# Performance work log

Measured on AMD Instinct MI355X. Metric: run time of the kernel, lower is better.

Reference implementation:

```python
import jax, jax.numpy as jnp
import numpy as np

N_NODES = 2000   # buses per graph = state_dim // 2
K_HOPS = 3       # TAGConv K
HIDDEN = 64
F_NODE = 2       # node_feat_dim
B_DIM, W_DIM = 8, 32


def setup_inputs() -> dict:
    key = jax.random.key(0)
    ks = jax.random.split(key, 4)
    N = N_NODES
    rng = np.random.default_rng(0)
    # sparse symmetric ybus sparsity: chain + random chords (power-grid like, avg degree ~4)
    ii = np.arange(N - 1)
    jj = ii + 1
    ci = np.arange(N)
    cj = (ci + rng.integers(2, N - 1, size=N)) % N
    src = np.concatenate([ii, ci])
    dst = np.concatenate([jj, cj])
    row = np.concatenate([src, dst]).astype(np.int32)   # symmetrized: both directions
    col = np.concatenate([dst, src]).astype(np.int32)
    w = rng.uniform(0.5, 2.0, size=src.shape[0]).astype(np.float32)  # |ybus| entries
    ew = np.concatenate([w, w]).astype(np.float32)
    x = jax.random.normal(ks[0], (B_DIM, W_DIM, 2 * N), dtype=jnp.float32)
    # TAGConv params: K+1 weight matrices (no per-lin bias in PyG TAGConv lins) + one bias
    W1 = jax.random.normal(ks[1], (K_HOPS + 1, F_NODE, HIDDEN), dtype=jnp.float32) * (1.0 / np.sqrt(F_NODE))
    b1 = jnp.zeros((HIDDEN,), jnp.float32)
    W2 = jax.random.normal(ks[2], (K_HOPS + 1, HIDDEN, F_NODE), dtype=jnp.float32) * (1.0 / np.sqrt(HIDDEN))
    b2 = jnp.zeros((F_NODE,), jnp.float32)
    return {"x": x, "row": jnp.asarray(row), "col": jnp.asarray(col),
            "ew": jnp.asarray(ew), "W1": W1, "b1": b1, "W2": W2, "b2": b2}


def _propagate(x, row, col, norm, N):
    # x: [G, N, F]; gather at source, weight, scatter-add at target
    msg = x[:, row, :] * norm[None, :, None]                       # [G, E, F]
    return jax.vmap(lambda m: jax.ops.segment_sum(m, col, num_segments=N))(msg)


def _tag_conv(x, Ws, b, row, col, norm, N):
    # TAGConv: out = sum_k lin_k(A_hat^k x) + b
    out = jnp.einsum('gnf,fo->gno', x, Ws[0])
    h = x
    for k in range(1, Ws.shape[0]):
        h = _propagate(h, row, col, norm, N)
        out = out + jnp.einsum('gnf,fo->gno', h, Ws[k])
    return out + b


def reference(x, row, col, ew, W1, b1, W2, b2):
    B, Wd, twoN = x.shape
    N = twoN // 2
    G = B * Wd
    xn = x.reshape(G, N, F_NODE)
    # gcn_norm (add_self_loops=False), shared across all tiled graphs
    deg = jax.ops.segment_sum(ew, col, num_segments=N)
    safe = jnp.where(deg > 0, deg, 1.0)
    dinv = jnp.where(deg > 0, 1.0 / jnp.sqrt(safe), 0.0)
    norm = dinv[row] * ew * dinv[col]
    h = _tag_conv(xn, W1, b1, row, col, norm, N)
    h = jax.nn.relu(h)
    h = _tag_conv(h, W2, b2, row, col, norm, N)
    out = xn + h  # residual refine
    return out.reshape(B, Wd, twoN)
```

## Files before the change

kernel.cpp:

```cpp
#include <hip/hip_runtime.h>
#include <math.h>


#define NN    2000
#define HID   64
#define TPB   1024
#define BKCAP 12

typedef float v2f __attribute__((ext_vector_type(2)));

struct NodeAdj {
    int   l, r, c;
    float wl, wr, wc;
    int   m0, m1, m2, m3;
    float w0, w1, w2, w3;
    int   tail0, tail1;
    float dn;
};

__device__ __forceinline__ v2f gather2(const v2f* __restrict__ buf,
                                       const NodeAdj& A,
                                       const unsigned short* __restrict__ bkt16,
                                       const float* __restrict__ ewc,
                                       const float* __restrict__ dinvL)
{
    v2f acc0 = A.wl * buf[A.l];
    v2f acc1 = A.wr * buf[A.r];
    acc0 += A.wc * buf[A.c];
    acc1 += A.w0 * buf[A.m0];
    acc0 += A.w1 * buf[A.m1];
    acc1 += A.w2 * buf[A.m2];
    acc0 += A.w3 * buf[A.m3];
    for (int p = A.tail0; p < A.tail1; ++p) {
        int m = bkt16[p];
        float w = A.dn * ewc[m] * dinvL[m];
        acc1 += w * buf[m];
    }
    return acc0 + acc1;
}

__global__ __launch_bounds__(TPB) void refine_kernel(
    const float* __restrict__ x,
    const int*   __restrict__ row, const int* __restrict__ col,
    const float* __restrict__ ew,
    const float* __restrict__ W1, const float* __restrict__ b1,
    const float* __restrict__ W2, const float* __restrict__ b2,
    float* __restrict__ out)
{
    __shared__ int            cnt[NN];
    __shared__ unsigned short bkt16[NN * BKCAP];
    __shared__ float          ewc[NN];
    __shared__ float          dinvL[NN];
    __shared__ v2f            bufP[NN];
    __shared__ v2f            bufQ[NN];

    const int g = blockIdx.x;
    const int t = threadIdx.x;
    const int n0 = t;
    const int n1 = t + TPB;
    const bool has1 = (n1 < NN);
    const float* xg   = x   + (size_t)g * (2 * NN);
    float*       outg = out + (size_t)g * (2 * NN);

    float y[2][8];
    v2f Zp[2][4];
#pragma unroll
    for (int q = 0; q < 8; ++q) { y[0][q] = 0.f; y[1][q] = 0.f; }
#pragma unroll
    for (int q = 0; q < 4; ++q) { Zp[0][q] = (v2f)0.f; Zp[1][q] = (v2f)0.f; }

    cnt[t] = 0;
    if (t + TPB < NN) cnt[t + TPB] = 0;
    ewc[n0] = ew[(NN - 1) + n0];
    if (has1) ewc[n1] = ew[(NN - 1) + n1];
    {
        v2f v = ((const v2f*)xg)[n0];
        bufP[n0] = v; y[0][0] = v.x; y[0][1] = v.y;
        if (has1) {
            v2f u = ((const v2f*)xg)[n1];
            bufP[n1] = u; y[1][0] = u.x; y[1][1] = u.y;
        }
    }
    const int cA = col[(NN - 1) + n0];
    const float ewlA = (n0 > 0)      ? ew[n0 - 1] : 0.f;
    const float ewrA = (n0 < NN - 1) ? ew[n0]     : 0.f;
    int cB = 0; float ewlB = 0.f, ewrB = 0.f;
    if (has1) {
        cB   = col[(NN - 1) + n1];
        ewlB = ew[n1 - 1];
        ewrB = (n1 < NN - 1) ? ew[n1] : 0.f;
    }
    __syncthreads();

    {
        int pos = atomicAdd(&cnt[cA], 1);
        if (pos < BKCAP) bkt16[cA * BKCAP + pos] = (unsigned short)n0;
        if (has1) {
            int pos1 = atomicAdd(&cnt[cB], 1);
            if (pos1 < BKCAP) bkt16[cB * BKCAP + pos1] = (unsigned short)n1;
        }
    }
    __syncthreads();

    int bdA = cnt[n0]; if (bdA > BKCAP) bdA = BKCAP;
    const int baseA = n0 * BKCAP;
    int mA0 = 0, mA1 = 0, mA2 = 0, mA3 = 0;
    float eA0 = 0.f, eA1 = 0.f, eA2 = 0.f, eA3 = 0.f;
    {
        float deg = ewc[n0] + ewlA + ewrA;
        if (bdA > 0) { mA0 = bkt16[baseA];     eA0 = ewc[mA0]; deg += eA0; }
        if (bdA > 1) { mA1 = bkt16[baseA + 1]; eA1 = ewc[mA1]; deg += eA1; }
        if (bdA > 2) { mA2 = bkt16[baseA + 2]; eA2 = ewc[mA2]; deg += eA2; }
        if (bdA > 3) { mA3 = bkt16[baseA + 3]; eA3 = ewc[mA3]; deg += eA3; }
        for (int k = 4; k < bdA; ++k) deg += ewc[bkt16[baseA + k]];
        dinvL[n0] = 1.0f / sqrtf(deg);
    }
    int bdB = 0, baseB = 0;
    int mB0 = 0, mB1 = 0, mB2 = 0, mB3 = 0;
    float eB0 = 0.f, eB1 = 0.f, eB2 = 0.f, eB3 = 0.f;
    if (has1) {
        bdB = cnt[n1]; if (bdB > BKCAP) bdB = BKCAP;
        baseB = n1 * BKCAP;
        float deg = ewc[n1] + ewlB + ewrB;
        if (bdB > 0) { mB0 = bkt16[baseB];     eB0 = ewc[mB0]; deg += eB0; }
        if (bdB > 1) { mB1 = bkt16[baseB + 1]; eB1 = ewc[mB1]; deg += eB1; }
        if (bdB > 2) { mB2 = bkt16[baseB + 2]; eB2 = ewc[mB2]; deg += eB2; }
        if (bdB > 3) { mB3 = bkt16[baseB + 3]; eB3 = ewc[mB3]; deg += eB3; }
        for (int k = 4; k < bdB; ++k) deg += ewc[bkt16[baseB + k]];
        dinvL[n1] = 1.0f / sqrtf(deg);
    }
    __syncthreads();

    NodeAdj A, B;
    {
        float dn = dinvL[n0];
        A.l = (n0 > 0) ? n0 - 1 : 0;
        A.r = (n0 < NN - 1) ? n0 + 1 : NN - 1;
        A.c = cA;
        A.wl = dn * ewlA * dinvL[A.l];
        A.wr = dn * ewrA * dinvL[A.r];
        A.wc = dn * ewc[n0] * dinvL[cA];
        A.m0 = mA0; A.m1 = mA1; A.m2 = mA2; A.m3 = mA3;
        A.w0 = dn * eA0 * dinvL[mA0];
        A.w1 = dn * eA1 * dinvL[mA1];
        A.w2 = dn * eA2 * dinvL[mA2];
        A.w3 = dn * eA3 * dinvL[mA3];
        A.tail0 = baseA + 4;
        A.tail1 = baseA + ((bdA > 4) ? bdA : 4);
        A.dn = dn;
    }
    B.l = 0; B.r = 0; B.c = 0; B.wl = 0.f; B.wr = 0.f; B.wc = 0.f;
    B.m0 = 0; B.m1 = 0; B.m2 = 0; B.m3 = 0;
    B.w0 = 0.f; B.w1 = 0.f; B.w2 = 0.f; B.w3 = 0.f;
    B.tail0 = 0; B.tail1 = 0; B.dn = 0.f;
    if (has1) {
        float dn = dinvL[n1];
        B.l = n1 - 1;
        B.r = (n1 < NN - 1) ? n1 + 1 : NN - 1;
        B.c = cB;
        B.wl = dn * ewlB * dinvL[B.l];
        B.wr = dn * ewrB * dinvL[B.r];
        B.wc = dn * ewc[n1] * dinvL[cB];
        B.m0 = mB0; B.m1 = mB1; B.m2 = mB2; B.m3 = mB3;
        B.w0 = dn * eB0 * dinvL[mB0];
        B.w1 = dn * eB1 * dinvL[mB1];
        B.w2 = dn * eB2 * dinvL[mB2];
        B.w3 = dn * eB3 * dinvL[mB3];
        B.tail0 = baseB + 4;
        B.tail1 = baseB + ((bdB > 4) ? bdB : 4);
        B.dn = dn;
    }

    v2f ra, rb;

    ra = gather2(bufP, A, bkt16, ewc, dinvL);
    if (has1) rb = gather2(bufP, B, bkt16, ewc, dinvL);
    y[0][2] = ra.x; y[0][3] = ra.y; bufQ[n0] = ra;
    if (has1) { y[1][2] = rb.x; y[1][3] = rb.y; bufQ[n1] = rb; }
    __syncthreads();

    ra = gather2(bufQ, A, bkt16, ewc, dinvL);
    if (has1) rb = gather2(bufQ, B, bkt16, ewc, dinvL);
    y[0][4] = ra.x; y[0][5] = ra.y; bufP[n0] = ra;
    if (has1) { y[1][4] = rb.x; y[1][5] = rb.y; bufP[n1] = rb; }
    __syncthreads();

    ra = gather2(bufP, A, bkt16, ewc, dinvL);
    if (has1) rb = gather2(bufP, B, bkt16, ewc, dinvL);
    y[0][6] = ra.x; y[0][7] = ra.y;
    if (has1) { y[1][6] = rb.x; y[1][7] = rb.y; }

    const v2f*    W1p = (const v2f*)W1;
    const v2f*    b1p = (const v2f*)b1;
    const float4* W2q = (const float4*)W2;
#pragma unroll 2
    for (int jh = 0; jh < HID / 2; ++jh) {
        v2f w1c[8];
#pragma unroll
        for (int m = 0; m < 8; ++m) w1c[m] = W1p[m * (HID / 2) + jh];
        v2f bj = b1p[jh];
        float4 w2a = W2q[0 * (HID / 2) + jh];
        float4 w2b = W2q[1 * (HID / 2) + jh];
        float4 w2c = W2q[2 * (HID / 2) + jh];
        float4 w2d = W2q[3 * (HID / 2) + jh];
        v2f wa_l = {w2a.x, w2a.y}, wa_h = {w2a.z, w2a.w};
        v2f wb_l = {w2b.x, w2b.y}, wb_h = {w2b.z, w2b.w};
        v2f wc_l = {w2c.x, w2c.y}, wc_h = {w2c.z, w2c.w};
        v2f wd_l = {w2d.x, w2d.y}, wd_h = {w2d.z, w2d.w};
#pragma unroll
        for (int i = 0; i < 2; ++i) {
            v2f ha = bj          + y[i][0] * w1c[0];
            v2f hb = y[i][1] * w1c[1] + y[i][2] * w1c[2];
            ha += y[i][3] * w1c[3];
            hb += y[i][4] * w1c[4];
            ha += y[i][5] * w1c[5];
            hb += y[i][6] * w1c[6];
            ha += y[i][7] * w1c[7];
            v2f h = ha + hb;
            float h0 = fmaxf(h.x, 0.f);
            float h1 = fmaxf(h.y, 0.f);
            Zp[i][0] += h0 * wa_l; Zp[i][0] += h1 * wa_h;
            Zp[i][1] += h0 * wb_l; Zp[i][1] += h1 * wb_h;
            Zp[i][2] += h0 * wc_l; Zp[i][2] += h1 * wc_h;
            Zp[i][3] += h0 * wd_l; Zp[i][3] += h1 * wd_h;
        }
    }

    bufQ[n0] = Zp[0][3];
    if (has1) bufQ[n1] = Zp[1][3];
    __syncthreads();

    ra = gather2(bufQ, A, bkt16, ewc, dinvL);
    if (has1) rb = gather2(bufQ, B, bkt16, ewc, dinvL);
    bufP[n0] = Zp[0][2] + ra;
    if (has1) bufP[n1] = Zp[1][2] + rb;
    __syncthreads();

    ra = gather2(bufP, A, bkt16, ewc, dinvL);
    if (has1) rb = gather2(bufP, B, bkt16, ewc, dinvL);
    bufQ[n0] = Zp[0][1] + ra;
    if (has1) bufQ[n1] = Zp[1][1] + rb;
    __syncthreads();

    const v2f b2v = {b2[0], b2[1]};
    ra = gather2(bufQ, A, bkt16, ewc, dinvL);
    if (has1) rb = gather2(bufQ, B, bkt16, ewc, dinvL);
    {
        v2f x0 = {y[0][0], y[0][1]};
        v2f o = x0 + b2v + Zp[0][0] + ra;
        ((v2f*)outg)[n0] = o;
        if (has1) {
            v2f x1 = {y[1][0], y[1][1]};
            v2f u = x1 + b2v + Zp[1][0] + rb;
            ((v2f*)outg)[n1] = u;
        }
    }
}

extern "C" void kernel_launch(void* const* d_in, const int* in_sizes, int n_in,
                              void* d_out, int out_size, void* d_ws, size_t ws_size,
                              hipStream_t stream) {
    const float* x   = (const float*)d_in[0];
    const int*   row = (const int*)  d_in[1];
    const int*   col = (const int*)  d_in[2];
    const float* ew  = (const float*)d_in[3];
    const float* W1  = (const float*)d_in[4];
    const float* b1  = (const float*)d_in[5];
    const float* W2  = (const float*)d_in[6];
    const float* b2  = (const float*)d_in[7];
    float* out = (float*)d_out;

    const int G = in_sizes[0] / (2 * NN);

    hipLaunchKernelGGL(refine_kernel, dim3(G), dim3(TPB), 0, stream,
                       x, row, col, ew, W1, b1, W2, b2, out);
}
```

Before: 102.5 us.

## Assign adjacent node pairs per thread with register-forwarded chain neighbours

Each thread now owns two adjacent nodes (2t, 2t+1) instead of nodes t and t+1024. The chain edge between the pair is served from registers (prevA/prevB), which removes one LDS gather per node per hop. Loads and stores of x, the buffers and the output widen to 16-byte vectors. In exchange, 1000 of 1024 threads are active, and the first-wave and second-wave workloads are no longer split, which may change latency hiding.

```diff
diff --git a/kernel.cpp b/kernel.cpp
--- a/kernel.cpp
+++ b/kernel.cpp
@@ -6,8 +6,10 @@
 #define HID   64
 #define TPB   1024
 #define BKCAP 12
+#define HALF  (NN / 2)
 
 typedef float v2f __attribute__((ext_vector_type(2)));
+typedef float v4f __attribute__((ext_vector_type(4)));
 
 struct NodeAdj {
     int   l, r, c;
@@ -18,25 +20,39 @@
     float dn;
 };
 
-__device__ __forceinline__ v2f gather2(const v2f* __restrict__ buf,
-                                       const NodeAdj& A,
-                                       const unsigned short* __restrict__ bkt16,
-                                       const float* __restrict__ ewc,
-                                       const float* __restrict__ dinvL)
+__device__ __forceinline__ void gatherPair(
+    const v2f* __restrict__ buf,
+    const NodeAdj& A, const NodeAdj& B,
+    v2f prevA, v2f prevB,
+    const unsigned short* __restrict__ bkt16,
+    const float* __restrict__ ewc,
+    const float* __restrict__ dinvL,
+    v2f& outA, v2f& outB)
 {
-    v2f acc0 = A.wl * buf[A.l];
-    v2f acc1 = A.wr * buf[A.r];
-    acc0 += A.wc * buf[A.c];
-    acc1 += A.w0 * buf[A.m0];
-    acc0 += A.w1 * buf[A.m1];
-    acc1 += A.w2 * buf[A.m2];
-    acc0 += A.w3 * buf[A.m3];
+    v2f a0 = A.wl * buf[A.l];
+    v2f a1 = A.wr * prevB;
+    v2f b0 = B.wl * prevA;
+    v2f b1 = B.wr * buf[B.r];
+    a0 += A.wc * buf[A.c];
+    b0 += B.wc * buf[B.c];
+    a1 += A.w0 * buf[A.m0];
+    b1 += B.w0 * buf[B.m0];
+    a0 += A.w1 * buf[A.m1];
+    b0 += B.w1 * buf[B.m1];
+    a1 += A.w2 * buf[A.m2];
+    b1 += B.w2 * buf[B.m2];
+    a0 += A.w3 * buf[A.m3];
+    b0 += B.w3 * buf[B.m3];
     for (int p = A.tail0; p < A.tail1; ++p) {
         int m = bkt16[p];
-        float w = A.dn * ewc[m] * dinvL[m];
-        acc1 += w * buf[m];
-    }
-    return acc0 + acc1;
+        a1 += (A.dn * ewc[m] * dinvL[m]) * buf[m];
+    }
+    for (int p = B.tail0; p < B.tail1; ++p) {
+        int m = bkt16[p];
+        b1 += (B.dn * ewc[m] * dinvL[m]) * buf[m];
+    }
+    outA = a0 + a1;
+    outB = b0 + b1;
 }
 
 __global__ __launch_bounds__(TPB) void refine_kernel(
@@ -47,18 +63,18 @@
     const float* __restrict__ W2, const float* __restrict__ b2,
     float* __restrict__ out)
 {
-    __shared__ int            cnt[NN];
-    __shared__ unsigned short bkt16[NN * BKCAP];
-    __shared__ float          ewc[NN];
-    __shared__ float          dinvL[NN];
-    __shared__ v2f            bufP[NN];
-    __shared__ v2f            bufQ[NN];
+    __shared__ int                          cnt[NN];
+    __shared__ unsigned short               bkt16[NN * BKCAP];
+    __shared__ __align__(16) float          ewc[NN];
+    __shared__ __align__(16) float          dinvL[NN];
+    __shared__ __align__(16) v2f            bufP[NN];
+    __shared__ __align__(16) v2f            bufQ[NN];
 
     const int g = blockIdx.x;
     const int t = threadIdx.x;
-    const int n0 = t;
-    const int n1 = t + TPB;
-    const bool has1 = (n1 < NN);
+    const bool act = (t < HALF);
+    const int n0 = 2 * t;
+    const int n1 = 2 * t + 1;
     const float* xg   = x   + (size_t)g * (2 * NN);
     float*       outg = out + (size_t)g * (2 * NN);
 
@@ -68,192 +84,197 @@
     for (int q = 0; q < 8; ++q) { y[0][q] = 0.f; y[1][q] = 0.f; }
 #pragma unroll
     for (int q = 0; q < 4; ++q) { Zp[0][q] = (v2f)0.f; Zp[1][q] = (v2f)0.f; }
+    v2f prevA = (v2f)0.f, prevB = (v2f)0.f;
 
     cnt[t] = 0;
     if (t + TPB < NN) cnt[t + TPB] = 0;
-    ewc[n0] = ew[(NN - 1) + n0];
-    if (has1) ewc[n1] = ew[(NN - 1) + n1];
-    {
-        v2f v = ((const v2f*)xg)[n0];
-        bufP[n0] = v; y[0][0] = v.x; y[0][1] = v.y;
-        if (has1) {
-            v2f u = ((const v2f*)xg)[n1];
-            bufP[n1] = u; y[1][0] = u.x; y[1][1] = u.y;
-        }
-    }
-    const int cA = col[(NN - 1) + n0];
-    const float ewlA = (n0 > 0)      ? ew[n0 - 1] : 0.f;
-    const float ewrA = (n0 < NN - 1) ? ew[n0]     : 0.f;
-    int cB = 0; float ewlB = 0.f, ewrB = 0.f;
-    if (has1) {
-        cB   = col[(NN - 1) + n1];
-        ewlB = ew[n1 - 1];
-        ewrB = (n1 < NN - 1) ? ew[n1] : 0.f;
-    }
-    __syncthreads();
-
-    {
+    int   cA = 0, cB = 0;
+    float ewl = 0.f, ewm = 0.f, ewr = 0.f;
+    float ecA = 0.f, ecB = 0.f;
+    if (act) {
+        ecA = ew[(NN - 1) + n0];
+        ecB = ew[(NN - 1) + n1];
+        ((float2*)ewc)[t] = make_float2(ecA, ecB);
+        v4f v = ((const v4f*)xg)[t];
+        ((v4f*)bufP)[t] = v;
+        y[0][0] = v.x; y[0][1] = v.y; y[1][0] = v.z; y[1][1] = v.w;
+        prevA = (v2f){v.x, v.y};
+        prevB = (v2f){v.z, v.w};
+        cA = col[(NN - 1) + n0];
+        cB = col[(NN - 1) + n1];
+        ewl = (n0 > 0) ? ew[n0 - 1] : 0.f;
+        ewm = ew[n0];
+        ewr = (n1 < NN - 1) ? ew[n1] : 0.f;
+    }
+    __syncthreads();
+
+    if (act) {
         int pos = atomicAdd(&cnt[cA], 1);
         if (pos < BKCAP) bkt16[cA * BKCAP + pos] = (unsigned short)n0;
-        if (has1) {
-            int pos1 = atomicAdd(&cnt[cB], 1);
-            if (pos1 < BKCAP) bkt16[cB * BKCAP + pos1] = (unsigned short)n1;
+        int pos1 = atomicAdd(&cnt[cB], 1);
+        if (pos1 < BKCAP) bkt16[cB * BKCAP + pos1] = (unsigned short)n1;
+    }
+    __syncthreads();
+
+    const int baseA = n0 * BKCAP, baseB = n1 * BKCAP;
+    int bdA = 0, bdB = 0;
+    int mA0 = 0, mA1 = 0, mA2 = 0, mA3 = 0;
+    int mB0 = 0, mB1 = 0, mB2 = 0, mB3 = 0;
+    float eA0 = 0.f, eA1 = 0.f, eA2 = 0.f, eA3 = 0.f;
+    float eB0 = 0.f, eB1 = 0.f, eB2 = 0.f, eB3 = 0.f;
+    float dnA = 0.f, dnB = 0.f;
+    if (act) {
+        bdA = cnt[n0]; if (bdA > BKCAP) bdA = BKCAP;
+        {
+            float deg = ecA + ewl + ewm;
+            if (bdA > 0) { mA0 = bkt16[baseA];     eA0 = ewc[mA0]; deg += eA0; }
+            if (bdA > 1) { mA1 = bkt16[baseA + 1]; eA1 = ewc[mA1]; deg += eA1; }
+            if (bdA > 2) { mA2 = bkt16[baseA + 2]; eA2 = ewc[mA2]; deg += eA2; }
+            if (bdA > 3) { mA3 = bkt16[baseA + 3]; eA3 = ewc[mA3]; deg += eA3; }
+            for (int k = 4; k < bdA; ++k) deg += ewc[bkt16[baseA + k]];
+            dnA = 1.0f / sqrtf(deg);
         }
-    }
-    __syncthreads();
-
-    int bdA = cnt[n0]; if (bdA > BKCAP) bdA = BKCAP;
-    const int baseA = n0 * BKCAP;
-    int mA0 = 0, mA1 = 0, mA2 = 0, mA3 = 0;
-    float eA0 = 0.f, eA1 = 0.f, eA2 = 0.f, eA3 = 0.f;
-    {
-        float deg = ewc[n0] + ewlA + ewrA;
-        if (bdA > 0) { mA0 = bkt16[baseA];     eA0 = ewc[mA0]; deg += eA0; }
-        if (bdA > 1) { mA1 = bkt16[baseA + 1]; eA1 = ewc[mA1]; deg += eA1; }
-        if (bdA > 2) { mA2 = bkt16[baseA + 2]; eA2 = ewc[mA2]; deg += eA2; }
-        if (bdA > 3) { mA3 = bkt16[baseA + 3]; eA3 = ewc[mA3]; deg += eA3; }
-        for (int k = 4; k < bdA; ++k) deg += ewc[bkt16[baseA + k]];
-        dinvL[n0] = 1.0f / sqrtf(deg);
-    }
-    int bdB = 0, baseB = 0;
-    int mB0 = 0, mB1 = 0, mB2 = 0, mB3 = 0;
-    float eB0 = 0.f, eB1 = 0.f, eB2 = 0.f, eB3 = 0.f;
-    if (has1) {
         bdB = cnt[n1]; if (bdB > BKCAP) bdB = BKCAP;
-        baseB = n1 * BKCAP;
-        float deg = ewc[n1] + ewlB + ewrB;
-        if (bdB > 0) { mB0 = bkt16[baseB];     eB0 = ewc[mB0]; deg += eB0; }
-        if (bdB > 1) { mB1 = bkt16[baseB + 1]; eB1 = ewc[mB1]; deg += eB1; }
-        if (bdB > 2) { mB2 = bkt16[baseB + 2]; eB2 = ewc[mB2]; deg += eB2; }
-        if (bdB > 3) { mB3 = bkt16[baseB + 3]; eB3 = ewc[mB3]; deg += eB3; }
-        for (int k = 4; k < bdB; ++k) deg += ewc[bkt16[baseB + k]];
-        dinvL[n1] = 1.0f / sqrtf(deg);
+        {
+            float deg = ecB + ewm + ewr;
+            if (bdB > 0) { mB0 = bkt16[baseB];     eB0 = ewc[mB0]; deg += eB0; }
+            if (bdB > 1) { mB1 = bkt16[baseB + 1]; eB1 = ewc[mB1]; deg += eB1; }
+            if (bdB > 2) { mB2 = bkt16[baseB + 2]; eB2 = ewc[mB2]; deg += eB2; }
+            if (bdB > 3) { mB3 = bkt16[baseB + 3]; eB3 = ewc[mB3]; deg += eB3; }
+            for (int k = 4; k < bdB; ++k) deg += ewc[bkt16[baseB + k]];
+            dnB = 1.0f / sqrtf(deg);
+        }
+        ((float2*)dinvL)[t] = make_float2(dnA, dnB);
     }
     __syncthreads();
 
     NodeAdj A, B;
-    {
-        float dn = dinvL[n0];
+    A.l = 0; A.r = 0; A.c = 0; A.wl = 0.f; A.wr = 0.f; A.wc = 0.f;
+    A.m0 = 0; A.m1 = 0; A.m2 = 0; A.m3 = 0;
+    A.w0 = 0.f; A.w1 = 0.f; A.w2 = 0.f; A.w3 = 0.f;
+    A.tail0 = 0; A.tail1 = 0; A.dn = 0.f;
+    B = A;
+    if (act) {
         A.l = (n0 > 0) ? n0 - 1 : 0;
-        A.r = (n0 < NN - 1) ? n0 + 1 : NN - 1;
         A.c = cA;
-        A.wl = dn * ewlA * dinvL[A.l];
-        A.wr = dn * ewrA * dinvL[A.r];
-        A.wc = dn * ewc[n0] * dinvL[cA];
+        A.wl = dnA * ewl * dinvL[A.l];
+        A.wr = dnA * ewm * dnB;
+        A.wc = dnA * ecA * dinvL[cA];
         A.m0 = mA0; A.m1 = mA1; A.m2 = mA2; A.m3 = mA3;
-        A.w0 = dn * eA0 * dinvL[mA0];
-        A.w1 = dn * eA1 * dinvL[mA1];
-        A.w2 = dn * eA2 * dinvL[mA2];
-        A.w3 = dn * eA3 * dinvL[mA3];
+        A.w0 = dnA * eA0 * dinvL[mA0];
+        A.w1 = dnA * eA1 * dinvL[mA1];
+        A.w2 = dnA * eA2 * dinvL[mA2];
+        A.w3 = dnA * eA3 * dinvL[mA3];
         A.tail0 = baseA + 4;
         A.tail1 = baseA + ((bdA > 4) ? bdA : 4);
-        A.dn = dn;
-    }
-    B.l = 0; B.r = 0; B.c = 0; B.wl = 0.f; B.wr = 0.f; B.wc = 0.f;
-    B.m0 = 0; B.m1 = 0; B.m2 = 0; B.m3 = 0;
-    B.w0 = 0.f; B.w1 = 0.f; B.w2 = 0.f; B.w3 = 0.f;
-    B.tail0 = 0; B.tail1 = 0; B.dn = 0.f;
-    if (has1) {
-        float dn = dinvL[n1];
-        B.l = n1 - 1;
+        A.dn = dnA;
+
         B.r = (n1 < NN - 1) ? n1 + 1 : NN - 1;
         B.c = cB;
-        B.wl = dn * ewlB * dinvL[B.l];
-        B.wr = dn * ewrB * dinvL[B.r];
-        B.wc = dn * ewc[n1] * dinvL[cB];
+        B.wl = dnB * ewm * dnA;
+        B.wr = dnB * ewr * dinvL[B.r];
+        B.wc = dnB * ecB * dinvL[cB];
         B.m0 = mB0; B.m1 = mB1; B.m2 = mB2; B.m3 = mB3;
-        B.w0 = dn * eB0 * dinvL[mB0];
-        B.w1 = dn * eB1 * dinvL[mB1];
-        B.w2 = dn * eB2 * dinvL[mB2];
-        B.w3 = dn * eB3 * dinvL[mB3];
+        B.w0 = dnB * eB0 * dinvL[mB0];
+        B.w1 = dnB * eB1 * dinvL[mB1];
+        B.w2 = dnB * eB2 * dinvL[mB2];
+        B.w3 = dnB * eB3 * dinvL[mB3];
         B.tail0 = baseB + 4;
         B.tail1 = baseB + ((bdB > 4) ? bdB : 4);
-        B.dn = dn;
+        B.dn = dnB;
     }
 
     v2f ra, rb;
 
-    ra = gather2(bufP, A, bkt16, ewc, dinvL);
-    if (has1) rb = gather2(bufP, B, bkt16, ewc, dinvL);
-    y[0][2] = ra.x; y[0][3] = ra.y; bufQ[n0] = ra;
-    if (has1) { y[1][2] = rb.x; y[1][3] = rb.y; bufQ[n1] = rb; }
-    __syncthreads();
-
-    ra = gather2(bufQ, A, bkt16, ewc, dinvL);
-    if (has1) rb = gather2(bufQ, B, bkt16, ewc, dinvL);
-    y[0][4] = ra.x; y[0][5] = ra.y; bufP[n0] = ra;
-    if (has1) { y[1][4] = rb.x; y[1][5] = rb.y; bufP[n1] = rb; }
-    __syncthreads();
-
-    ra = gather2(bufP, A, bkt16, ewc, dinvL);
-    if (has1) rb = gather2(bufP, B, bkt16, ewc, dinvL);
-    y[0][6] = ra.x; y[0][7] = ra.y;
-    if (has1) { y[1][6] = rb.x; y[1][7] = rb.y; }
-
-    const v2f*    W1p = (const v2f*)W1;
-    const v2f*    b1p = (const v2f*)b1;
-    const float4* W2q = (const float4*)W2;
+    if (act) {
+        gatherPair(bufP, A, B, prevA, prevB, bkt16, ewc, dinvL, ra, rb);
+        y[0][2] = ra.x; y[0][3] = ra.y; y[1][2] = rb.x; y[1][3] = rb.y;
+        ((v4f*)bufQ)[t] = (v4f){ra.x, ra.y, rb.x, rb.y};
+        prevA = ra; prevB = rb;
+    }
+    __syncthreads();
+
+    if (act) {
+        gatherPair(bufQ, A, B, prevA, prevB, bkt16, ewc, dinvL, ra, rb);
+        y[0][4] = ra.x; y[0][5] = ra.y; y[1][4] = rb.x; y[1][5] = rb.y;
+        ((v4f*)bufP)[t] = (v4f){ra.x, ra.y, rb.x, rb.y};
+        prevA = ra; prevB = rb;
+    }
+    __syncthreads();
+
+    if (act) {
+        gatherPair(bufP, A, B, prevA, prevB, bkt16, ewc, dinvL, ra, rb);
+        y[0][6] = ra.x; y[0][7] = ra.y; y[1][6] = rb.x; y[1][7] = rb.y;
+    }
+
+    if (act) {
+        const v2f*    W1p = (const v2f*)W1;
+        const v2f*    b1p = (const v2f*)b1;
+        const float4* W2q = (const float4*)W2;
 #pragma unroll 2
-    for (int jh = 0; jh < HID / 2; ++jh) {
-        v2f w1c[8];
-#pragma unroll
-        for (int m = 0; m < 8; ++m) w1c[m] = W1p[m * (HID / 2) + jh];
-        v2f bj = b1p[jh];
-        float4 w2a = W2q[0 * (HID / 2) + jh];
-        float4 w2b = W2q[1 * (HID / 2) + jh];
-        float4 w2c = W2q[2 * (HID / 2) + jh];
-        float4 w2d = W2q[3 * (HID / 2) + jh];
-        v2f wa_l = {w2a.x, w2a.y}, wa_h = {w2a.z, w2a.w};
-        v2f wb_l = {w2b.x, w2b.y}, wb_h = {w2b.z, w2b.w};
-        v2f wc_l = {w2c.x, w2c.y}, wc_h = {w2c.z, w2c.w};
-        v2f wd_l = {w2d.x, w2d.y}, wd_h = {w2d.z, w2d.w};
-#pragma unroll
-        for (int i = 0; i < 2; ++i) {
-            v2f ha = bj          + y[i][0] * w1c[0];
-            v2f hb = y[i][1] * w1c[1] + y[i][2] * w1c[2];
-            ha += y[i][3] * w1c[3];
-            hb += y[i][4] * w1c[4];
-            ha += y[i][5] * w1c[5];
-            hb += y[i][6] * w1c[6];
-            ha += y[i][7] * w1c[7];
-            v2f h = ha + hb;
-            float h0 = fmaxf(h.x, 0.f);
-            float h1 = fmaxf(h.y, 0.f);
-            Zp[i][0] += h0 * wa_l; Zp[i][0] += h1 * wa_h;
-            Zp[i][1] += h0 * wb_l; Zp[i][1] += h1 * wb_h;
-            Zp[i][2] += h0 * wc_l; Zp[i][2] += h1 * wc_h;
-            Zp[i][3] += h0 * wd_l; Zp[i][3] += h1 * wd_h;
+        for (int jh = 0; jh < HID / 2; ++jh) {
+            v2f w1c[8];
+#pragma unroll
+            for (int m = 0; m < 8; ++m) w1c[m] = W1p[m * (HID / 2) + jh];
+            v2f bj = b1p[jh];
+            float4 w2a = W2q[0 * (HID / 2) + jh];
+            float4 w2b = W2q[1 * (HID / 2) + jh];
+            float4 w2c = W2q[2 * (HID / 2) + jh];
+            float4 w2d = W2q[3 * (HID / 2) + jh];
+            v2f wa_l = {w2a.x, w2a.y}, wa_h = {w2a.z, w2a.w};
+            v2f wb_l = {w2b.x, w2b.y}, wb_h = {w2b.z, w2b.w};
+            v2f wc_l = {w2c.x, w2c.y}, wc_h = {w2c.z, w2c.w};
+            v2f wd_l = {w2d.x, w2d.y}, wd_h = {w2d.z, w2d.w};
+#pragma unroll
+            for (int i = 0; i < 2; ++i) {
+                v2f ha = bj          + y[i][0] * w1c[0];
+                v2f hb = y[i][1] * w1c[1] + y[i][2] * w1c[2];
+                ha += y[i][3] * w1c[3];
+                hb += y[i][4] * w1c[4];
+                ha += y[i][5] * w1c[5];
+                hb += y[i][6] * w1c[6];
+                ha += y[i][7] * w1c[7];
+                v2f h = ha + hb;
+                float h0 = fmaxf(h.x, 0.f);
+                float h1 = fmaxf(h.y, 0.f);
+                Zp[i][0] += h0 * wa_l; Zp[i][0] += h1 * wa_h;
+                Zp[i][1] += h0 * wb_l; Zp[i][1] += h1 * wb_h;
+                Zp[i][2] += h0 * wc_l; Zp[i][2] += h1 * wc_h;
+                Zp[i][3] += h0 * wd_l; Zp[i][3] += h1 * wd_h;
+            }
         }
     }
 
-    bufQ[n0] = Zp[0][3];
-    if (has1) bufQ[n1] = Zp[1][3];
-    __syncthreads();
-
-    ra = gather2(bufQ, A, bkt16, ewc, dinvL);
-    if (has1) rb = gather2(bufQ, B, bkt16, ewc, dinvL);
-    bufP[n0] = Zp[0][2] + ra;
-    if (has1) bufP[n1] = Zp[1][2] + rb;
-    __syncthreads();
-
-    ra = gather2(bufP, A, bkt16, ewc, dinvL);
-    if (has1) rb = gather2(bufP, B, bkt16, ewc, dinvL);
-    bufQ[n0] = Zp[0][1] + ra;
-    if (has1) bufQ[n1] = Zp[1][1] + rb;
-    __syncthreads();
-
-    const v2f b2v = {b2[0], b2[1]};
-    ra = gather2(bufQ, A, bkt16, ewc, dinvL);
-    if (has1) rb = gather2(bufQ, B, bkt16, ewc, dinvL);
-    {
+    if (act) {
+        ((v4f*)bufQ)[t] = (v4f){Zp[0][3].x, Zp[0][3].y, Zp[1][3].x, Zp[1][3].y};
+        prevA = Zp[0][3]; prevB = Zp[1][3];
+    }
+    __syncthreads();
+
+    if (act) {
+        gatherPair(bufQ, A, B, prevA, prevB, bkt16, ewc, dinvL, ra, rb);
+        v2f sA = Zp[0][2] + ra, sB = Zp[1][2] + rb;
+        ((v4f*)bufP)[t] = (v4f){sA.x, sA.y, sB.x, sB.y};
+        prevA = sA; prevB = sB;
+    }
+    __syncthreads();
+
+    if (act) {
+        gatherPair(bufP, A, B, prevA, prevB, bkt16, ewc, dinvL, ra, rb);
+        v2f sA = Zp[0][1] + ra, sB = Zp[1][1] + rb;
+        ((v4f*)bufQ)[t] = (v4f){sA.x, sA.y, sB.x, sB.y};
+        prevA = sA; prevB = sB;
+    }
+    __syncthreads();
+
+    if (act) {
+        const v2f b2v = {b2[0], b2[1]};
+        gatherPair(bufQ, A, B, prevA, prevB, bkt16, ewc, dinvL, ra, rb);
         v2f x0 = {y[0][0], y[0][1]};
-        v2f o = x0 + b2v + Zp[0][0] + ra;
-        ((v2f*)outg)[n0] = o;
-        if (has1) {
-            v2f x1 = {y[1][0], y[1][1]};
-            v2f u = x1 + b2v + Zp[1][0] + rb;
-            ((v2f*)outg)[n1] = u;
-        }
+        v2f x1 = {y[1][0], y[1][1]};
+        v2f oA = x0 + b2v + Zp[0][0] + ra;
+        v2f oB = x1 + b2v + Zp[1][0] + rb;
+        ((v4f*)outg)[t] = (v4f){oA.x, oA.y, oB.x, oB.y};
     }
 }
 
```

Result: slower. 112.4 us (+9.7%).

## Precompute normalized adjacency once in a separate build kernel

Applied to the files above, without the earlier changes.

Before this change, each of the 256 graph blocks rebuilt the bucketed adjacency and gcn normalization in large shared memory. Now a single-block build kernel writes packed per-node neighbor indices and weights to workspace. The refine kernel then only loads them as float4/int4 and keeps small shared buffers. This removes redundant per-block setup and shrinks LDS use, which may allow more blocks per CU. The cost is an extra serial kernel launch and global reads in the tail loop.

```diff
diff --git a/kernel.cpp b/kernel.cpp
--- a/kernel.cpp
+++ b/kernel.cpp
@@ -11,18 +11,16 @@
 
 struct NodeAdj {
     int   l, r, c;
+    int   m0, m1, m2, m3;
     float wl, wr, wc;
-    int   m0, m1, m2, m3;
     float w0, w1, w2, w3;
-    int   tail0, tail1;
-    float dn;
+    int   tbase, tc;
 };
 
 __device__ __forceinline__ v2f gather2(const v2f* __restrict__ buf,
                                        const NodeAdj& A,
-                                       const unsigned short* __restrict__ bkt16,
-                                       const float* __restrict__ ewc,
-                                       const float* __restrict__ dinvL)
+                                       const int* __restrict__ adjtm,
+                                       const float* __restrict__ adjtw)
 {
     v2f acc0 = A.wl * buf[A.l];
     v2f acc1 = A.wr * buf[A.r];
@@ -31,56 +29,33 @@
     acc0 += A.w1 * buf[A.m1];
     acc1 += A.w2 * buf[A.m2];
     acc0 += A.w3 * buf[A.m3];
-    for (int p = A.tail0; p < A.tail1; ++p) {
-        int m = bkt16[p];
-        float w = A.dn * ewc[m] * dinvL[m];
+    for (int p = 0; p < A.tc; ++p) {
+        int   m = adjtm[A.tbase + p];
+        float w = adjtw[A.tbase + p];
         acc1 += w * buf[m];
     }
     return acc0 + acc1;
 }
 
-__global__ __launch_bounds__(TPB) void refine_kernel(
-    const float* __restrict__ x,
-    const int*   __restrict__ row, const int* __restrict__ col,
-    const float* __restrict__ ew,
-    const float* __restrict__ W1, const float* __restrict__ b1,
-    const float* __restrict__ W2, const float* __restrict__ b2,
-    float* __restrict__ out)
+__global__ __launch_bounds__(TPB) void build_kernel(
+    const int* __restrict__ col, const float* __restrict__ ew,
+    float* __restrict__ adjw, int* __restrict__ adji,
+    float* __restrict__ adjtw, int* __restrict__ adjtm)
 {
     __shared__ int            cnt[NN];
     __shared__ unsigned short bkt16[NN * BKCAP];
     __shared__ float          ewc[NN];
     __shared__ float          dinvL[NN];
-    __shared__ v2f            bufP[NN];
-    __shared__ v2f            bufQ[NN];
-
-    const int g = blockIdx.x;
+
     const int t = threadIdx.x;
     const int n0 = t;
     const int n1 = t + TPB;
     const bool has1 = (n1 < NN);
-    const float* xg   = x   + (size_t)g * (2 * NN);
-    float*       outg = out + (size_t)g * (2 * NN);
-
-    float y[2][8];
-    v2f Zp[2][4];
-#pragma unroll
-    for (int q = 0; q < 8; ++q) { y[0][q] = 0.f; y[1][q] = 0.f; }
-#pragma unroll
-    for (int q = 0; q < 4; ++q) { Zp[0][q] = (v2f)0.f; Zp[1][q] = (v2f)0.f; }
 
     cnt[t] = 0;
     if (t + TPB < NN) cnt[t + TPB] = 0;
     ewc[n0] = ew[(NN - 1) + n0];
     if (has1) ewc[n1] = ew[(NN - 1) + n1];
-    {
-        v2f v = ((const v2f*)xg)[n0];
-        bufP[n0] = v; y[0][0] = v.x; y[0][1] = v.y;
-        if (has1) {
-            v2f u = ((const v2f*)xg)[n1];
-            bufP[n1] = u; y[1][0] = u.x; y[1][1] = u.y;
-        }
-    }
     const int cA = col[(NN - 1) + n0];
     const float ewlA = (n0 > 0)      ? ew[n0 - 1] : 0.f;
     const float ewrA = (n0 < NN - 1) ? ew[n0]     : 0.f;
@@ -131,62 +106,135 @@
     }
     __syncthreads();
 
+    {
+        float dn = dinvL[n0];
+        int l = (n0 > 0) ? n0 - 1 : 0;
+        int r = (n0 < NN - 1) ? n0 + 1 : NN - 1;
+        float4* wp = (float4*)(adjw + n0 * 8);
+        wp[0] = make_float4(dn * ewlA * dinvL[l],
+                            dn * ewrA * dinvL[r],
+                            dn * ewc[n0] * dinvL[cA],
+                            dn * eA0 * dinvL[mA0]);
+        wp[1] = make_float4(dn * eA1 * dinvL[mA1],
+                            dn * eA2 * dinvL[mA2],
+                            dn * eA3 * dinvL[mA3], 0.f);
+        int4* ip = (int4*)(adji + n0 * 8);
+        ip[0] = make_int4(cA, mA0, mA1, mA2);
+        ip[1] = make_int4(mA3, bdA, 0, 0);
+        int tc = (bdA > 4) ? bdA - 4 : 0;
+        for (int k = 0; k < tc; ++k) {
+            int m = bkt16[baseA + 4 + k];
+            adjtm[n0 * 8 + k] = m;
+            adjtw[n0 * 8 + k] = dn * ewc[m] * dinvL[m];
+        }
+    }
+    if (has1) {
+        float dn = dinvL[n1];
+        int l = n1 - 1;
+        int r = (n1 < NN - 1) ? n1 + 1 : NN - 1;
+        float4* wp = (float4*)(adjw + n1 * 8);
+        wp[0] = make_float4(dn * ewlB * dinvL[l],
+                            dn * ewrB * dinvL[r],
+                            dn * ewc[n1] * dinvL[cB],
+                            dn * eB0 * dinvL[mB0]);
+        wp[1] = make_float4(dn * eB1 * dinvL[mB1],
+                            dn * eB2 * dinvL[mB2],
+                            dn * eB3 * dinvL[mB3], 0.f);
+        int4* ip = (int4*)(adji + n1 * 8);
+        ip[0] = make_int4(cB, mB0, mB1, mB2);
+        ip[1] = make_int4(mB3, bdB, 0, 0);
+        int tc = (bdB > 4) ? bdB - 4 : 0;
+        for (int k = 0; k < tc; ++k) {
+            int m = bkt16[baseB + 4 + k];
+            adjtm[n1 * 8 + k] = m;
+            adjtw[n1 * 8 + k] = dn * ewc[m] * dinvL[m];
+        }
+    }
+}
+
+__global__ __launch_bounds__(TPB) void refine_kernel(
+    const float* __restrict__ x,
+    const float* __restrict__ W1, const float* __restrict__ b1,
+    const float* __restrict__ W2, const float* __restrict__ b2,
+    const float* __restrict__ adjw, const int* __restrict__ adji,
+    const float* __restrict__ adjtw, const int* __restrict__ adjtm,
+    float* __restrict__ out)
+{
+    __shared__ v2f bufP[NN];
+    __shared__ v2f bufQ[NN];
+
+    const int g = blockIdx.x;
+    const int t = threadIdx.x;
+    const int n0 = t;
+    const int n1 = t + TPB;
+    const bool has1 = (n1 < NN);
+    const float* xg   = x   + (size_t)g * (2 * NN);
+    float*       outg = out + (size_t)g * (2 * NN);
+
+    float y[2][8];
+    v2f Zp[2][4];
+#pragma unroll
+    for (int q = 0; q < 8; ++q) { y[0][q] = 0.f; y[1][q] = 0.f; }
+#pragma unroll
+    for (int q = 0; q < 4; ++q) { Zp[0][q] = (v2f)0.f; Zp[1][q] = (v2f)0.f; }
+
+    {
+        v2f v = ((const v2f*)xg)[n0];
+        bufP[n0] = v; y[0][0] = v.x; y[0][1] = v.y;
+        if (has1) {
+            v2f u = ((const v2f*)xg)[n1];
+            bufP[n1] = u; y[1][0] = u.x; y[1][1] = u.y;
+        }
+    }
     NodeAdj A, B;
     {
-        float dn = dinvL[n0];
+        float4 w0 = ((const float4*)(adjw))[n0 * 2];
+        float4 w1 = ((const float4*)(adjw))[n0 * 2 + 1];
+        int4   i0 = ((const int4*)(adji))[n0 * 2];
+        int4   i1 = ((const int4*)(adji))[n0 * 2 + 1];
         A.l = (n0 > 0) ? n0 - 1 : 0;
         A.r = (n0 < NN - 1) ? n0 + 1 : NN - 1;
-        A.c = cA;
-        A.wl = dn * ewlA * dinvL[A.l];
-        A.wr = dn * ewrA * dinvL[A.r];
-        A.wc = dn * ewc[n0] * dinvL[cA];
-        A.m0 = mA0; A.m1 = mA1; A.m2 = mA2; A.m3 = mA3;
-        A.w0 = dn * eA0 * dinvL[mA0];
-        A.w1 = dn * eA1 * dinvL[mA1];
-        A.w2 = dn * eA2 * dinvL[mA2];
-        A.w3 = dn * eA3 * dinvL[mA3];
-        A.tail0 = baseA + 4;
-        A.tail1 = baseA + ((bdA > 4) ? bdA : 4);
-        A.dn = dn;
-    }
-    B.l = 0; B.r = 0; B.c = 0; B.wl = 0.f; B.wr = 0.f; B.wc = 0.f;
-    B.m0 = 0; B.m1 = 0; B.m2 = 0; B.m3 = 0;
+        A.c = i0.x; A.m0 = i0.y; A.m1 = i0.z; A.m2 = i0.w; A.m3 = i1.x;
+        A.wl = w0.x; A.wr = w0.y; A.wc = w0.z; A.w0 = w0.w;
+        A.w1 = w1.x; A.w2 = w1.y; A.w3 = w1.z;
+        A.tbase = n0 * 8;
+        A.tc = (i1.y > 4) ? i1.y - 4 : 0;
+    }
+    B.l = 0; B.r = 0; B.c = 0; B.m0 = 0; B.m1 = 0; B.m2 = 0; B.m3 = 0;
+    B.wl = 0.f; B.wr = 0.f; B.wc = 0.f;
     B.w0 = 0.f; B.w1 = 0.f; B.w2 = 0.f; B.w3 = 0.f;
-    B.tail0 = 0; B.tail1 = 0; B.dn = 0.f;
+    B.tbase = 0; B.tc = 0;
     if (has1) {
-        float dn = dinvL[n1];
+        float4 w0 = ((const float4*)(adjw))[n1 * 2];
+        float4 w1 = ((const float4*)(adjw))[n1 * 2 + 1];
+        int4   i0 = ((const int4*)(adji))[n1 * 2];
+        int4   i1 = ((const int4*)(adji))[n1 * 2 + 1];
         B.l = n1 - 1;
         B.r = (n1 < NN - 1) ? n1 + 1 : NN - 1;
-        B.c = cB;
-        B.wl = dn * ewlB * dinvL[B.l];
-        B.wr = dn * ewrB * dinvL[B.r];
-        B.wc = dn * ewc[n1] * dinvL[cB];
-        B.m0 = mB0; B.m1 = mB1; B.m2 = mB2; B.m3 = mB3;
-        B.w0 = dn * eB0 * dinvL[mB0];
-        B.w1 = dn * eB1 * dinvL[mB1];
-        B.w2 = dn * eB2 * dinvL[mB2];
-        B.w3 = dn * eB3 * dinvL[mB3];
-        B.tail0 = baseB + 4;
-        B.tail1 = baseB + ((bdB > 4) ? bdB : 4);
-        B.dn = dn;
-    }
+        B.c = i0.x; B.m0 = i0.y; B.m1 = i0.z; B.m2 = i0.w; B.m3 = i1.x;
+        B.wl = w0.x; B.wr = w0.y; B.wc = w0.z; B.w0 = w0.w;
+        B.w1 = w1.x; B.w2 = w1.y; B.w3 = w1.z;
+        B.tbase = n1 * 8;
+        B.tc = (i1.y > 4) ? i1.y - 4 : 0;
+    }
+    __syncthreads();
 
     v2f ra, rb;
 
-    ra = gather2(bufP, A, bkt16, ewc, dinvL);
-    if (has1) rb = gather2(bufP, B, bkt16, ewc, dinvL);
+    ra = gather2(bufP, A, adjtm, adjtw);
+    if (has1) rb = gather2(bufP, B, adjtm, adjtw);
     y[0][2] = ra.x; y[0][3] = ra.y; bufQ[n0] = ra;
     if (has1) { y[1][2] = rb.x; y[1][3] = rb.y; bufQ[n1] = rb; }
     __syncthreads();
 
-    ra = gather2(bufQ, A, bkt16, ewc, dinvL);
-    if (has1) rb = gather2(bufQ, B, bkt16, ewc, dinvL);
+    ra = gather2(bufQ, A, adjtm, adjtw);
+    if (has1) rb = gather2(bufQ, B, adjtm, adjtw);
     y[0][4] = ra.x; y[0][5] = ra.y; bufP[n0] = ra;
     if (has1) { y[1][4] = rb.x; y[1][5] = rb.y; bufP[n1] = rb; }
     __syncthreads();
 
-    ra = gather2(bufP, A, bkt16, ewc, dinvL);
-    if (has1) rb = gather2(bufP, B, bkt16, ewc, dinvL);
+    ra = gather2(bufP, A, adjtm, adjtw);
+    if (has1) rb = gather2(bufP, B, adjtm, adjtw);
     y[0][6] = ra.x; y[0][7] = ra.y;
     if (has1) { y[1][6] = rb.x; y[1][7] = rb.y; }
 
@@ -230,21 +278,21 @@
     if (has1) bufQ[n1] = Zp[1][3];
     __syncthreads();
 
-    ra = gather2(bufQ, A, bkt16, ewc, dinvL);
-    if (has1) rb = gather2(bufQ, B, bkt16, ewc, dinvL);
+    ra = gather2(bufQ, A, adjtm, adjtw);
+    if (has1) rb = gather2(bufQ, B, adjtm, adjtw);
     bufP[n0] = Zp[0][2] + ra;
     if (has1) bufP[n1] = Zp[1][2] + rb;
     __syncthreads();
 
-    ra = gather2(bufP, A, bkt16, ewc, dinvL);
-    if (has1) rb = gather2(bufP, B, bkt16, ewc, dinvL);
+    ra = gather2(bufP, A, adjtm, adjtw);
+    if (has1) rb = gather2(bufP, B, adjtm, adjtw);
     bufQ[n0] = Zp[0][1] + ra;
     if (has1) bufQ[n1] = Zp[1][1] + rb;
     __syncthreads();
 
     const v2f b2v = {b2[0], b2[1]};
-    ra = gather2(bufQ, A, bkt16, ewc, dinvL);
-    if (has1) rb = gather2(bufQ, B, bkt16, ewc, dinvL);
+    ra = gather2(bufQ, A, adjtm, adjtw);
+    if (has1) rb = gather2(bufQ, B, adjtm, adjtw);
     {
         v2f x0 = {y[0][0], y[0][1]};
         v2f o = x0 + b2v + Zp[0][0] + ra;
@@ -261,7 +309,6 @@
                               void* d_out, int out_size, void* d_ws, size_t ws_size,
                               hipStream_t stream) {
     const float* x   = (const float*)d_in[0];
-    const int*   row = (const int*)  d_in[1];
     const int*   col = (const int*)  d_in[2];
     const float* ew  = (const float*)d_in[3];
     const float* W1  = (const float*)d_in[4];
@@ -270,8 +317,15 @@
     const float* b2  = (const float*)d_in[7];
     float* out = (float*)d_out;
 
+    float* adjw  = (float*)d_ws;
+    int*   adji  = (int*)  ((char*)d_ws + 64000);
+    float* adjtw = (float*)((char*)d_ws + 128000);
+    int*   adjtm = (int*)  ((char*)d_ws + 192000);
+
     const int G = in_sizes[0] / (2 * NN);
 
+    hipLaunchKernelGGL(build_kernel, dim3(1), dim3(TPB), 0, stream,
+                       col, ew, adjw, adji, adjtw, adjtm);
     hipLaunchKernelGGL(refine_kernel, dim3(G), dim3(TPB), 0, stream,
-                       x, row, col, ew, W1, b1, W2, b2, out);
+                       x, W1, b1, W2, b2, adjw, adji, adjtw, adjtm, out);
 }
```

Result: faster. 91.84 us (median of 2 runs) (-10.4%).
